# Kernel optimization log

Measured on AMD Instinct MI355X. Metric: run time of the kernel, lower is better.

The kernel has to match this reference:

```python
import jax, jax.numpy as jnp
import numpy as np

RADIUS = 2                 # soft detection radius (init kwarg)
NMS_RADIUS = 2             # hardcoded in detect_keypoints: simple_nms(scores, 2)
TOP_K = 4096
TEMPERATURE = 0.1
KSIZE = 2 * RADIUS + 1     # 5
KK = KSIZE * KSIZE         # 25


def _hw_grid(dtype):
    # flatten order j = dy*KSIZE + dx ; entry = (x_off, y_off)  (torch's [:, [1,0]])
    lin = jnp.linspace(-RADIUS, RADIUS, KSIZE, dtype=dtype)
    gx, gy = jnp.meshgrid(lin, lin)  # 'xy': gx[dy,dx]=lin[dx], gy[dy,dx]=lin[dy]
    return jnp.stack([gx, gy], axis=-1).reshape(-1, 2)  # (KK, 2)


def _maxpool(x, r):
    k = 2 * r + 1
    return jax.lax.reduce_window(x, -jnp.inf, jax.lax.max,
                                 (1, 1, k, k), (1, 1, 1, 1),
                                 ((0, 0), (0, 0), (r, r), (r, r)))


def _simple_nms(scores, r):
    zeros = jnp.zeros_like(scores)
    max_mask = scores == _maxpool(scores, r)
    for _ in range(2):
        supp_mask = _maxpool(max_mask.astype(scores.dtype), r) > 0
        supp_scores = jnp.where(supp_mask, zeros, scores)
        new_max_mask = supp_scores == _maxpool(supp_scores, r)
        max_mask = max_mask | (new_max_mask & ~supp_mask)
    return jnp.where(max_mask, scores, zeros)


def _bilinear_zeros(img, xy):
    # img: (h, w); xy: (K, 2) normalized [-1,1]; align_corners=True, zero padding
    h, w = img.shape
    px = (xy[:, 0] + 1.0) * 0.5 * (w - 1)
    py = (xy[:, 1] + 1.0) * 0.5 * (h - 1)
    x0 = jnp.floor(px); y0 = jnp.floor(py)
    wx1 = px - x0; wx0 = 1.0 - wx1
    wy1 = py - y0; wy0 = 1.0 - wy1
    def tap(xi, yi, wgt):
        valid = (xi >= 0) & (xi < w) & (yi >= 0) & (yi < h)
        xc = jnp.clip(xi, 0, w - 1).astype(jnp.int32)
        yc = jnp.clip(yi, 0, h - 1).astype(jnp.int32)
        return jnp.where(valid, img[yc, xc], 0.0) * wgt
    return (tap(x0, y0, wx0 * wy0) + tap(x0 + 1, y0, wx1 * wy0)
            + tap(x0, y0 + 1, wx0 * wy1) + tap(x0 + 1, y0 + 1, wx1 * wy1))


def _dkd_forward(scores_map):
    b, c, h, w = scores_map.shape
    dtype = scores_map.dtype
    scores_nograd = jax.lax.stop_gradient(scores_map)

    nms_scores = _simple_nms(scores_nograd, NMS_RADIUS)
    # zero out border band of width RADIUS
    ybad = (jnp.arange(h) < RADIUS) | (jnp.arange(h) >= h - RADIUS)
    xbad = (jnp.arange(w) < RADIUS) | (jnp.arange(w) >= w - RADIUS)
    border = ybad[:, None] | xbad[None, :]
    nms_scores = jnp.where(border[None, None], 0.0, nms_scores)

    # top-k over flattened score map (per image)
    _, idx = jax.lax.top_k(nms_scores.reshape(b, -1), TOP_K)  # (b, K)
    ix = idx % w
    iy = idx // w

    # patch gather == unfold(scores_map) + gather, done sparsely with zero pad
    padded = jnp.pad(scores_map[:, 0], ((0, 0), (RADIUS, RADIUS), (RADIUS, RADIUS)))
    off = jnp.arange(KSIZE)
    ys = iy[:, :, None] + off[None, None, :]           # (b, K, KSIZE)
    xs = ix[:, :, None] + off[None, None, :]
    bidx = jnp.arange(b)[:, None, None, None]
    patch_scores = padded[bidx, ys[:, :, :, None], xs[:, :, None, :]]  # (b,K,KSIZE,KSIZE)
    patch_scores = patch_scores.reshape(b, TOP_K, KK)

    hw_grid = _hw_grid(dtype)                          # (KK, 2)
    max_v = jax.lax.stop_gradient(patch_scores.max(axis=-1, keepdims=True))
    x_exp = jnp.exp((patch_scores - max_v) / TEMPERATURE)   # (b,K,KK)
    x_exp_sum = x_exp.sum(axis=-1, keepdims=True)            # (b,K,1)
    xy_residual = jnp.einsum('bkp,pd->bkd', x_exp, hw_grid) / x_exp_sum  # (b,K,2)
    hw_dist2 = (((hw_grid[None, None] - xy_residual[:, :, None]) / RADIUS) ** 2).sum(-1)
    scoredispersity = (x_exp * hw_dist2).sum(-1) / x_exp_sum[..., 0]     # (b,K)

    keypoints_xy_nms = jnp.stack([ix, iy], axis=-1).astype(dtype)
    wh = jnp.array([w - 1, h - 1], dtype=dtype)
    keypoints_xy = (keypoints_xy_nms + xy_residual) / wh * 2.0 - 1.0     # (b,K,2)

    kptscore = jax.vmap(_bilinear_zeros)(scores_map[:, 0], keypoints_xy)  # (b,K)
    return keypoints_xy, kptscore, scoredispersity


def setup_inputs() -> dict:
    key = jax.random.key(0)
    scores_map = jax.random.uniform(key, (8, 1, 1024, 1024), dtype=jnp.float32)
    return {"scores_map": scores_map}


def reference(scores_map):
    # matches torch forward: (keypoints, kptscores, scoredispersitys)
    return _dkd_forward(scores_map)
```

## Files before the change

kernel.cpp:

```cpp
#include <hip/hip_runtime.h>
#include <stdint.h>


namespace {

constexpr int B = 8;
constexpr int H = 1024;
constexpr int W = 1024;
constexpr int TOPK = 4096;
constexpr int CAND_CAP = 131072;
constexpr int SEL_CAP = 16384;
constexpr int LIST_CAP = 320;
constexpr int NHB = 32;

constexpr int RROWS = 92;
constexpr int NG = 22;
constexpr int STR = 88;
constexpr int MW4 = 4;
constexpr int NSTRIP = 11;
constexpr int NUNIT = NG * NSTRIP;

constexpr int RK_ME = 256;
constexpr int RK_CH = 1024;

constexpr size_t OFF_CNT   = 0;
constexpr size_t OFF_EH    = 4096;
constexpr size_t OFF_FH    = OFF_EH + (size_t)B * 256 * 4;
constexpr size_t OFF_RANK  = OFF_FH + (size_t)B * 256 * 4;
constexpr size_t OFF_SEL   = OFF_RANK + (size_t)B * SEL_CAP * 4;
constexpr size_t OFF_TOPK  = OFF_SEL + (size_t)B * SEL_CAP * 8;
constexpr size_t OFF_CAND  = OFF_TOPK + (size_t)B * TOPK * 8;
constexpr size_t MEMSET_BYTES = OFF_SEL;

__device__ __forceinline__ float max5(float a, float b, float c, float d, float e) {
  return fmaxf(fmaxf(fmaxf(a, b), fmaxf(c, d)), e);
}
__device__ __forceinline__ float4 ld4(const float* p) {
  return *reinterpret_cast<const float4*>(p);
}

template <int PASS>
__device__ __forceinline__ void score_pass(
    int u, int x0, int y0, const float* __restrict__ S,
    const uint32_t* __restrict__ MIN_, uint32_t* __restrict__ MOUT,
    uint64_t* list, uint32_t* cnt_loc, uint64_t* cand, uint32_t* cand_count, int b) {
  const int G = u % NG, s = u / NG;
  const int r0 = 2 + 8 * s;
  const int gx0 = x0 - 12 + 4 * G;
  uint32_t colm = 0;
#pragma unroll
  for (int j = 0; j < 4; ++j)
    if ((unsigned)(gx0 + j) < (unsigned)W) colm |= 1u << j;

  const int p2 = 4 * G - 6;
  const int pw2 = (p2 < 0) ? 0 : (p2 >> 5);
  const int psh2 = (p2 < 0) ? 0 : (p2 & 31);
  const int pls2 = (p2 < 0) ? -p2 : 0;

  float4 hw[5], cw[5];
  uint32_t snr[5], mor[5], cnb[5];
  constexpr int NK = (PASS == 0) ? 12 : 16;
#pragma unroll
  for (int k = 0; k < NK; ++k) {
    if (PASS != 0) {
      const int mr = r0 - 4 + k;
      uint32_t morrow = 0, cnib = 0;
      if ((unsigned)mr < (unsigned)RROWS) {
        const uint32_t* srow = MIN_ + mr * MW4;
        uint64_t X = (uint64_t)srow[pw2] | ((uint64_t)srow[pw2 + 1] << 32);
        uint64_t win = pls2 ? (X << pls2) : (X >> psh2);
        uint64_t t5 = win | (win >> 1) | (win >> 2) | (win >> 3) | (win >> 4);
        morrow = (uint32_t)t5 & 0xFFFu;
        cnib = (uint32_t)(win >> 6) & 0xFu;
      }
      mor[k % 5] = morrow;
      cnb[k % 5] = cnib;
    }
    const int ks = (PASS == 0) ? k : k - 4;
    if (ks >= 0) {
      const int sr = r0 - 2 + ks;
      uint32_t supp = 0;
      if (PASS != 0) supp = mor[0] | mor[1] | mor[2] | mor[3] | mor[4];
      const float* rowp = S + sr * STR + 4 * G;
      float4 d = ld4(rowp);
      float4 a = (G > 0) ? ld4(rowp - 4) : d;
      float4 e = (G < NG - 1) ? ld4(rowp + 4) : d;
      if (PASS != 0) {
        if (supp & 0x001u) a.x = 0.f;
        if (supp & 0x002u) a.y = 0.f;
        if (supp & 0x004u) a.z = 0.f;
        if (supp & 0x008u) a.w = 0.f;
        if (supp & 0x010u) d.x = 0.f;
        if (supp & 0x020u) d.y = 0.f;
        if (supp & 0x040u) d.z = 0.f;
        if (supp & 0x080u) d.w = 0.f;
        if (supp & 0x100u) e.x = 0.f;
        if (supp & 0x200u) e.y = 0.f;
        if (supp & 0x400u) e.z = 0.f;
        if (supp & 0x800u) e.w = 0.f;
      }
      float4 hm;
      hm.x = max5(a.z, a.w, d.x, d.y, d.z);
      hm.y = max5(a.w, d.x, d.y, d.z, d.w);
      hm.z = max5(d.x, d.y, d.z, d.w, e.x);
      hm.w = max5(d.y, d.z, d.w, e.x, e.y);
      hw[ks % 5] = hm;
      cw[ks % 5] = d;
      snr[ks % 5] = (supp >> 4) & 0xFu;
      if (ks >= 4) {
        const int rq = r0 - 4 + ks;
        const int gy = y0 - 12 + rq;
        float4 vm;
        vm.x = max5(hw[0].x, hw[1].x, hw[2].x, hw[3].x, hw[4].x);
        vm.y = max5(hw[0].y, hw[1].y, hw[2].y, hw[3].y, hw[4].y);
        vm.z = max5(hw[0].z, hw[1].z, hw[2].z, hw[3].z, hw[4].z);
        vm.w = max5(hw[0].w, hw[1].w, hw[2].w, hw[3].w, hw[4].w);
        float4 c = cw[(ks + 3) % 5];
        uint32_t nm = (uint32_t)(c.x == vm.x) | ((uint32_t)(c.y == vm.y) << 1) |
                      ((uint32_t)(c.z == vm.z) << 2) | ((uint32_t)(c.w == vm.w) << 3);
        nm &= ((unsigned)gy < (unsigned)H) ? colm : 0u;
        const int widx = rq * MW4 + (G >> 3);
        const int shift = 4 * (G & 7);
        if (PASS == 0) {
          if (nm) atomicOr(&MOUT[widx], nm << shift);
        } else if (PASS == 1) {
          uint32_t fin = cnb[ks % 5] | (nm & ~snr[(ks + 3) % 5]);
          if (fin) atomicOr(&MOUT[widx], fin << shift);
        } else {
          uint32_t fin = cnb[ks % 5] | (nm & ~snr[(ks + 3) % 5]);
          if (fin && G >= 3 && G < 19 && rq >= 12 && rq < 76 && gy >= 2 && gy < H - 2) {
#pragma unroll
            for (int j = 0; j < 4; ++j) {
              if ((fin >> j) & 1u) {
                int gx = gx0 + j;
                if (gx >= 2 && gx < W - 2) {
                  float sval = S[rq * STR + 4 * G + j];
                  if (sval > 0.0f) {
                    uint32_t bits = __float_as_uint(sval);
                    uint32_t flat = (uint32_t)(gy * W + gx);
                    uint64_t key = ((uint64_t)bits << 32) | (uint64_t)(0xFFFFFFFFu - flat);
                    uint32_t pos = atomicAdd(cnt_loc, 1u);
                    if (pos < (uint32_t)LIST_CAP) {
                      list[pos] = key;
                    } else {
                      uint32_t pp = atomicAdd(&cand_count[b], 1u);
                      if (pp < (uint32_t)CAND_CAP) cand[(size_t)b * CAND_CAP + pp] = key;
                    }
                  }
                }
              }
            }
          }
        }
      }
    }
  }
}

__global__ void __launch_bounds__(256, 4) k_nms(const float* __restrict__ scores,
                                                uint64_t* __restrict__ cand,
                                                uint32_t* __restrict__ cand_count) {
  __shared__ float S[RROWS * STR];
  __shared__ uint32_t M0s[RROWS * MW4];
  __shared__ uint32_t M1s[RROWS * MW4];
  __shared__ uint64_t list[LIST_CAP];
  __shared__ uint32_t cnt_loc, base_g;
  const int b = blockIdx.z;
  const int x0 = blockIdx.x * 64, y0 = blockIdx.y * 64;
  const int tid = threadIdx.x;
  const float* img = scores + (size_t)b * H * W;
  if (tid == 0) cnt_loc = 0;

  for (int u = tid; u < RROWS * NG; u += 256) {
    int r = u / NG, G = u % NG;
    int gy = y0 - 12 + r, gx = x0 - 12 + 4 * G;
    float4 v;
    if ((unsigned)gy < (unsigned)H && (unsigned)gx < (unsigned)W)
      v = ld4(img + (size_t)gy * W + gx);
    else
      v = make_float4(-INFINITY, -INFINITY, -INFINITY, -INFINITY);
    *reinterpret_cast<float4*>(&S[r * STR + 4 * G]) = v;
  }
  for (int i = tid; i < RROWS * MW4; i += 256) {
    M0s[i] = 0;
    M1s[i] = 0;
  }
  __syncthreads();
  if (tid < NUNIT)
    score_pass<0>(tid, x0, y0, S, nullptr, M0s, nullptr, nullptr, nullptr, nullptr, b);
  __syncthreads();
  if (tid < NUNIT)
    score_pass<1>(tid, x0, y0, S, M0s, M1s, nullptr, nullptr, nullptr, nullptr, b);
  __syncthreads();
  if (tid < NUNIT)
    score_pass<2>(tid, x0, y0, S, M1s, nullptr, list, &cnt_loc, cand, cand_count, b);
  __syncthreads();
  uint32_t nblk = cnt_loc;
  uint32_t nmain = nblk < (uint32_t)LIST_CAP ? nblk : (uint32_t)LIST_CAP;
  if (tid == 0) base_g = atomicAdd(&cand_count[b], nmain);
  __syncthreads();
  uint32_t bg = base_g;
  for (uint32_t i = tid; i < nmain; i += 256) {
    uint32_t pp = bg + i;
    if (pp < (uint32_t)CAND_CAP) cand[(size_t)b * CAND_CAP + pp] = list[i];
  }
}

__global__ void __launch_bounds__(256) k_ehist(const uint64_t* __restrict__ cand,
                                               const uint32_t* __restrict__ cand_count,
                                               uint32_t* __restrict__ gehist) {
  __shared__ uint32_t eh[256];
  const int b = blockIdx.y;
  uint32_t n = cand_count[b];
  if (n > (uint32_t)CAND_CAP) n = CAND_CAP;
  eh[threadIdx.x] = 0;
  __syncthreads();
  const uint64_t* cb = cand + (size_t)b * CAND_CAP;
  for (uint32_t i = blockIdx.x * 256 + threadIdx.x; i < n; i += NHB * 256)
    atomicAdd(&eh[(uint32_t)(cb[i] >> 55)], 1u);
  __syncthreads();
  uint32_t v = eh[threadIdx.x];
  if (v) atomicAdd(&gehist[b * 256 + threadIdx.x], v);
}

__global__ void __launch_bounds__(256) k_fhist(const uint64_t* __restrict__ cand,
                                               const uint32_t* __restrict__ cand_count,
                                               const uint32_t* __restrict__ gehist,
                                               uint32_t* __restrict__ gfhist) {
  __shared__ uint32_t fh[256];
  __shared__ uint32_t ehl[256];
  __shared__ int sE;
  const int b = blockIdx.y, t = threadIdx.x;
  uint32_t n = cand_count[b];
  if (n > (uint32_t)CAND_CAP) n = CAND_CAP;
  fh[t] = 0;
  ehl[t] = gehist[b * 256 + t];
  __syncthreads();
  if (t == 0) {
    uint32_t run = 0;
    int E = -1;
    for (int e = 255; e >= 0; --e) {
      uint32_t nrun = run + ehl[e];
      if (run < (uint32_t)TOPK && nrun >= (uint32_t)TOPK) E = e;
      run = nrun;
    }
    if (run < (uint32_t)TOPK) E = -1;
    sE = E;
  }
  __syncthreads();
  const int E = sE;
  if (E < 0) return;
  const uint64_t* cb = cand + (size_t)b * CAND_CAP;
  for (uint32_t i = blockIdx.x * 256 + t; i < n; i += NHB * 256) {
    uint64_t key = cb[i];
    if ((uint32_t)(key >> 55) == (uint32_t)E)
      atomicAdd(&fh[(uint32_t)(key >> 47) & 0xFFu], 1u);
  }
  __syncthreads();
  uint32_t v = fh[t];
  if (v) atomicAdd(&gfhist[b * 256 + t], v);
}

__global__ void __launch_bounds__(256) k_findthr(const uint32_t* __restrict__ gehist,
                                                 const uint32_t* __restrict__ gfhist,
                                                 uint64_t* __restrict__ thr_key) {
  __shared__ uint32_t ehl[256];
  __shared__ uint32_t fhl[256];
  const int b = blockIdx.x, t = threadIdx.x;
  ehl[t] = gehist[b * 256 + t];
  fhl[t] = gfhist[b * 256 + t];
  __syncthreads();
  if (t != 0) return;
  uint32_t run = 0, above = 0;
  int E = -1;
  for (int e = 255; e >= 0; --e) {
    uint32_t nrun = run + ehl[e];
    if (run < (uint32_t)TOPK && nrun >= (uint32_t)TOPK) {
      E = e;
      above = run;
    }
    run = nrun;
  }
  if (run < (uint32_t)TOPK) {
    thr_key[b] = 0ull;
    return;
  }
  uint32_t r2 = above;
  for (int j = 255; j >= 0; --j) {
    r2 += fhl[j];
    if (r2 >= (uint32_t)TOPK) {
      thr_key[b] = ((uint64_t)(((uint32_t)E << 8) | (uint32_t)j)) << 47;
      return;
    }
  }
}

__global__ void __launch_bounds__(1024) k_compact(const uint64_t* __restrict__ cand,
                                                  const uint32_t* __restrict__ cand_count,
                                                  const uint64_t* __restrict__ thr_key,
                                                  uint64_t* __restrict__ sel,
                                                  uint32_t* __restrict__ sel_count) {
  __shared__ uint64_t list[1024];
  __shared__ uint32_t cnt_loc;
  __shared__ uint32_t base_g;
  const int b = blockIdx.y;
  uint32_t n = cand_count[b];
  if (n > (uint32_t)CAND_CAP) n = CAND_CAP;
  const int tid = threadIdx.x;
  if (tid == 0) cnt_loc = 0;
  __syncthreads();
  uint32_t i = blockIdx.x * 1024 + tid;
  if (i < n) {
    uint64_t key = cand[(size_t)b * CAND_CAP + i];
    if (key >= thr_key[b]) {
      uint32_t pos = atomicAdd(&cnt_loc, 1u);
      list[pos] = key;
    }
  }
  __syncthreads();
  uint32_t nblk = cnt_loc;
  if (tid == 0 && nblk > 0) base_g = atomicAdd(&sel_count[b], nblk);
  __syncthreads();
  if (nblk > 0 && (uint32_t)tid < nblk) {
    uint32_t pp = base_g + tid;
    if (pp < (uint32_t)SEL_CAP) sel[(size_t)b * SEL_CAP + pp] = list[tid];
  }
}

__global__ void __launch_bounds__(RK_ME) k_rank_part(const uint64_t* __restrict__ sel,
                                                     const uint32_t* __restrict__ sel_count,
                                                     uint32_t* __restrict__ rankg) {
  __shared__ uint64_t keys[RK_CH];
  const int b = blockIdx.z;
  uint32_t n = sel_count[b];
  if (n > (uint32_t)SEL_CAP) n = SEL_CAP;
  const uint32_t me0 = blockIdx.x * RK_ME;
  const uint32_t c0 = blockIdx.y * RK_CH;
  if (me0 >= n || c0 >= n) return;
  const uint64_t* sb = sel + (size_t)b * SEL_CAP;
  uint32_t clen = n - c0;
  if (clen > (uint32_t)RK_CH) clen = RK_CH;
  for (uint32_t i = threadIdx.x; i < clen; i += RK_ME) keys[i] = sb[c0 + i];
  __syncthreads();
  const uint32_t me = me0 + threadIdx.x;
  if (me >= n) return;
  const uint64_t kme = sb[me];
  uint32_t rank = 0;
  uint32_t i = 0;
  for (; i + 8 <= clen; i += 8) {
    rank += (keys[i] > kme);
    rank += (keys[i + 1] > kme);
    rank += (keys[i + 2] > kme);
    rank += (keys[i + 3] > kme);
    rank += (keys[i + 4] > kme);
    rank += (keys[i + 5] > kme);
    rank += (keys[i + 6] > kme);
    rank += (keys[i + 7] > kme);
  }
  for (; i < clen; ++i) rank += (keys[i] > kme);
  if (rank) atomicAdd(&rankg[(size_t)b * SEL_CAP + me], rank);
}

__global__ void __launch_bounds__(256) k_scatter(const uint64_t* __restrict__ sel,
                                                 const uint32_t* __restrict__ sel_count,
                                                 const uint32_t* __restrict__ rankg,
                                                 uint64_t* __restrict__ topk) {
  const int b = blockIdx.y;
  uint32_t n = sel_count[b];
  if (n > (uint32_t)SEL_CAP) n = SEL_CAP;
  uint32_t i = blockIdx.x * 256 + threadIdx.x;
  if (i >= n) return;
  uint32_t r = rankg[(size_t)b * SEL_CAP + i];
  if (r < (uint32_t)TOPK) topk[(size_t)b * TOPK + r] = sel[(size_t)b * SEL_CAP + i];
}

__global__ void __launch_bounds__(256) k_refine(const float* __restrict__ scores,
                                                const uint64_t* __restrict__ topk,
                                                float* __restrict__ out) {
  int gid = blockIdx.x * 256 + threadIdx.x;
  int kp = gid >> 3, ln = gid & 7;
  const int b = kp / TOPK;
  const int k = kp % TOPK;
  uint64_t key = topk[(size_t)b * TOPK + k];
  uint32_t flat = 0xFFFFFFFFu - (uint32_t)(key & 0xFFFFFFFFull);
  if (flat >= (uint32_t)(H * W)) flat = 0;
  const int ix = (int)(flat % W);
  const int iy = (int)(flat / W);
  const float* img = scores + (size_t)b * H * W;

  const int nt = (ln == 0) ? 4 : 3;
  float v[4];
  float mymax = -INFINITY;
#pragma unroll
  for (int i = 0; i < 4; ++i) {
    if (i < nt) {
      int t = ln + 8 * i;
      int y = iy + t / 5 - 2, x = ix + t % 5 - 2;
      float val = ((unsigned)x < (unsigned)W && (unsigned)y < (unsigned)H)
                      ? img[(size_t)y * W + x] : 0.0f;
      v[i] = val;
      mymax = fmaxf(mymax, val);
    }
  }
#pragma unroll
  for (int m = 1; m < 8; m <<= 1) mymax = fmaxf(mymax, __shfl_xor(mymax, m));
  float e[4];
  float sum = 0.f, sx = 0.f, sy = 0.f;
#pragma unroll
  for (int i = 0; i < 4; ++i) {
    if (i < nt) {
      int t = ln + 8 * i;
      float ev = expf((v[i] - mymax) / 0.1f);
      e[i] = ev;
      sum += ev;
      sx += ev * (float)(t % 5 - 2);
      sy += ev * (float)(t / 5 - 2);
    }
  }
#pragma unroll
  for (int m = 1; m < 8; m <<= 1) {
    sum += __shfl_xor(sum, m);
    sx += __shfl_xor(sx, m);
    sy += __shfl_xor(sy, m);
  }
  float rx = sx / sum, ry = sy / sum;
  float dsp = 0.f;
#pragma unroll
  for (int i = 0; i < 4; ++i) {
    if (i < nt) {
      int t = ln + 8 * i;
      float dx = ((float)(t % 5 - 2) - rx) * 0.5f;
      float dy = ((float)(t / 5 - 2) - ry) * 0.5f;
      dsp += e[i] * (dx * dx + dy * dy);
    }
  }
#pragma unroll
  for (int m = 1; m < 8; m <<= 1) dsp += __shfl_xor(dsp, m);
  if (ln != 0) return;
  dsp /= sum;
  float kx = ((float)ix + rx) / 1023.0f * 2.0f - 1.0f;
  float ky = ((float)iy + ry) / 1023.0f * 2.0f - 1.0f;
  float px = (kx + 1.0f) * 0.5f * 1023.0f;
  float py = (ky + 1.0f) * 0.5f * 1023.0f;
  float x0f = floorf(px), y0f = floorf(py);
  float wx1 = px - x0f, wx0 = 1.0f - wx1;
  float wy1 = py - y0f, wy0 = 1.0f - wy1;
  int x0 = (int)x0f, y0 = (int)y0f;
  float sc = 0.0f;
  {
    int xs[2] = {x0, x0 + 1};
    int ys[2] = {y0, y0 + 1};
    float wxs[2] = {wx0, wx1};
    float wys[2] = {wy0, wy1};
#pragma unroll
    for (int yy = 0; yy < 2; ++yy)
#pragma unroll
      for (int xx = 0; xx < 2; ++xx) {
        int xi = xs[xx], yi = ys[yy];
        bool valid = (xi >= 0 && xi < W && yi >= 0 && yi < H);
        int xc = min(max(xi, 0), W - 1);
        int yc = min(max(yi, 0), H - 1);
        float vv = valid ? img[(size_t)yc * W + xc] : 0.0f;
        sc += vv * (wxs[xx] * wys[yy]);
      }
  }
  out[((size_t)b * TOPK + k) * 2 + 0] = kx;
  out[((size_t)b * TOPK + k) * 2 + 1] = ky;
  out[(size_t)B * TOPK * 2 + (size_t)b * TOPK + k] = sc;
  out[(size_t)B * TOPK * 3 + (size_t)b * TOPK + k] = dsp;
}

}

extern "C" void kernel_launch(void* const* d_in, const int* in_sizes, int n_in,
                              void* d_out, int out_size, void* d_ws, size_t ws_size,
                              hipStream_t stream) {
  const float* scores = (const float*)d_in[0];
  float* out = (float*)d_out;
  char* ws = (char*)d_ws;

  uint32_t* cnt = (uint32_t*)(ws + OFF_CNT);
  uint32_t* cand_count = cnt;
  uint32_t* sel_count  = cnt + 8;
  uint64_t* thr_key    = (uint64_t*)(cnt + 16);
  uint32_t* gehist = (uint32_t*)(ws + OFF_EH);
  uint32_t* gfhist = (uint32_t*)(ws + OFF_FH);
  uint32_t* rankg = (uint32_t*)(ws + OFF_RANK);
  uint64_t* sel  = (uint64_t*)(ws + OFF_SEL);
  uint64_t* topk = (uint64_t*)(ws + OFF_TOPK);
  uint64_t* cand = (uint64_t*)(ws + OFF_CAND);

  hipMemsetAsync(ws + OFF_CNT, 0, MEMSET_BYTES, stream);

  k_nms<<<dim3(W / 64, H / 64, B), 256, 0, stream>>>(scores, cand, cand_count);
  k_ehist<<<dim3(NHB, B), 256, 0, stream>>>(cand, cand_count, gehist);
  k_fhist<<<dim3(NHB, B), 256, 0, stream>>>(cand, cand_count, gehist, gfhist);
  k_findthr<<<B, 256, 0, stream>>>(gehist, gfhist, thr_key);
  k_compact<<<dim3(CAND_CAP / 1024, B), 1024, 0, stream>>>(cand, cand_count, thr_key,
                                                           sel, sel_count);
  k_rank_part<<<dim3(SEL_CAP / RK_ME, SEL_CAP / RK_CH, B), RK_ME, 0, stream>>>(
      sel, sel_count, rankg);
  k_scatter<<<dim3(SEL_CAP / 256, B), 256, 0, stream>>>(sel, sel_count, rankg, topk);
  k_refine<<<(B * TOPK * 8) / 256, 256, 0, stream>>>(scores, topk, out);
}
```

Before: 208.4 us.

## Fuse threshold search into compaction and scatter into refine, shrink memset

Drops the single-threaded k_findthr kernel. k_compact now loads both histograms and finds the threshold key with a parallel shared-memory suffix scan. Drops k_scatter: k_refine iterates over the selected list, reads each key's rank and writes its output at that rank. rankg is now zeroed inside compaction instead of by the memset, so the memset covers fewer bytes, and shared mask rows are padded from 4 to 5 words. This removes two launches and a global round-trip, at the cost of launching refine over the full selection capacity with many early-exit threads and repeating the scan in every compact block.

Result: faster. 198.7 us (-4.6%).

```diff
diff --git a/kernel.cpp b/kernel.cpp
--- a/kernel.cpp
+++ b/kernel.cpp
@@ -1,6 +1,5 @@
 #include <hip/hip_runtime.h>
 #include <stdint.h>
-
 
 namespace {
 
@@ -16,7 +15,7 @@
 constexpr int RROWS = 92;
 constexpr int NG = 22;
 constexpr int STR = 88;
-constexpr int MW4 = 4;
+constexpr int MW = 5;
 constexpr int NSTRIP = 11;
 constexpr int NUNIT = NG * NSTRIP;
 
@@ -28,9 +27,8 @@
 constexpr size_t OFF_FH    = OFF_EH + (size_t)B * 256 * 4;
 constexpr size_t OFF_RANK  = OFF_FH + (size_t)B * 256 * 4;
 constexpr size_t OFF_SEL   = OFF_RANK + (size_t)B * SEL_CAP * 4;
-constexpr size_t OFF_TOPK  = OFF_SEL + (size_t)B * SEL_CAP * 8;
-constexpr size_t OFF_CAND  = OFF_TOPK + (size_t)B * TOPK * 8;
-constexpr size_t MEMSET_BYTES = OFF_SEL;
+constexpr size_t OFF_CAND  = OFF_SEL + (size_t)B * SEL_CAP * 8;
+constexpr size_t MEMSET_BYTES = OFF_RANK;
 
 __device__ __forceinline__ float max5(float a, float b, float c, float d, float e) {
   return fmaxf(fmaxf(fmaxf(a, b), fmaxf(c, d)), e);
@@ -66,7 +64,7 @@
       const int mr = r0 - 4 + k;
       uint32_t morrow = 0, cnib = 0;
       if ((unsigned)mr < (unsigned)RROWS) {
-        const uint32_t* srow = MIN_ + mr * MW4;
+        const uint32_t* srow = MIN_ + mr * MW;
         uint64_t X = (uint64_t)srow[pw2] | ((uint64_t)srow[pw2 + 1] << 32);
         uint64_t win = pls2 ? (X << pls2) : (X >> psh2);
         uint64_t t5 = win | (win >> 1) | (win >> 2) | (win >> 3) | (win >> 4);
@@ -119,7 +117,7 @@
         uint32_t nm = (uint32_t)(c.x == vm.x) | ((uint32_t)(c.y == vm.y) << 1) |
                       ((uint32_t)(c.z == vm.z) << 2) | ((uint32_t)(c.w == vm.w) << 3);
         nm &= ((unsigned)gy < (unsigned)H) ? colm : 0u;
-        const int widx = rq * MW4 + (G >> 3);
+        const int widx = rq * MW + (G >> 3);
         const int shift = 4 * (G & 7);
         if (PASS == 0) {
           if (nm) atomicOr(&MOUT[widx], nm << shift);
@@ -161,8 +159,8 @@
                                                 uint64_t* __restrict__ cand,
                                                 uint32_t* __restrict__ cand_count) {
   __shared__ float S[RROWS * STR];
-  __shared__ uint32_t M0s[RROWS * MW4];
-  __shared__ uint32_t M1s[RROWS * MW4];
+  __shared__ uint32_t M0s[RROWS * MW];
+  __shared__ uint32_t M1s[RROWS * MW];
   __shared__ uint64_t list[LIST_CAP];
   __shared__ uint32_t cnt_loc, base_g;
   const int b = blockIdx.z;
@@ -181,7 +179,7 @@
       v = make_float4(-INFINITY, -INFINITY, -INFINITY, -INFINITY);
     *reinterpret_cast<float4*>(&S[r * STR + 4 * G]) = v;
   }
-  for (int i = tid; i < RROWS * MW4; i += 256) {
+  for (int i = tid; i < RROWS * MW; i += 256) {
     M0s[i] = 0;
     M1s[i] = 0;
   }
@@ -261,58 +259,66 @@
   if (v) atomicAdd(&gfhist[b * 256 + t], v);
 }
 
-__global__ void __launch_bounds__(256) k_findthr(const uint32_t* __restrict__ gehist,
-                                                 const uint32_t* __restrict__ gfhist,
-                                                 uint64_t* __restrict__ thr_key) {
-  __shared__ uint32_t ehl[256];
-  __shared__ uint32_t fhl[256];
-  const int b = blockIdx.x, t = threadIdx.x;
-  ehl[t] = gehist[b * 256 + t];
-  fhl[t] = gfhist[b * 256 + t];
-  __syncthreads();
-  if (t != 0) return;
-  uint32_t run = 0, above = 0;
-  int E = -1;
-  for (int e = 255; e >= 0; --e) {
-    uint32_t nrun = run + ehl[e];
-    if (run < (uint32_t)TOPK && nrun >= (uint32_t)TOPK) {
-      E = e;
-      above = run;
-    }
-    run = nrun;
-  }
-  if (run < (uint32_t)TOPK) {
-    thr_key[b] = 0ull;
-    return;
-  }
-  uint32_t r2 = above;
-  for (int j = 255; j >= 0; --j) {
-    r2 += fhl[j];
-    if (r2 >= (uint32_t)TOPK) {
-      thr_key[b] = ((uint64_t)(((uint32_t)E << 8) | (uint32_t)j)) << 47;
-      return;
-    }
-  }
-}
-
 __global__ void __launch_bounds__(1024) k_compact(const uint64_t* __restrict__ cand,
                                                   const uint32_t* __restrict__ cand_count,
-                                                  const uint64_t* __restrict__ thr_key,
+                                                  const uint32_t* __restrict__ gehist,
+                                                  const uint32_t* __restrict__ gfhist,
                                                   uint64_t* __restrict__ sel,
-                                                  uint32_t* __restrict__ sel_count) {
+                                                  uint32_t* __restrict__ sel_count,
+                                                  uint32_t* __restrict__ rankg) {
   __shared__ uint64_t list[1024];
-  __shared__ uint32_t cnt_loc;
-  __shared__ uint32_t base_g;
+  __shared__ uint32_t cnt_loc, base_g;
+  __shared__ uint32_t eh[256], fh[256];
+  __shared__ int sE;
+  __shared__ uint32_t sAbove;
+  __shared__ uint64_t s_thr;
   const int b = blockIdx.y;
   uint32_t n = cand_count[b];
   if (n > (uint32_t)CAND_CAP) n = CAND_CAP;
   const int tid = threadIdx.x;
-  if (tid == 0) cnt_loc = 0;
-  __syncthreads();
+  if (tid == 0) {
+    cnt_loc = 0;
+    sE = -1;
+    s_thr = 0ull;
+  }
+  if (tid < 256) {
+    eh[tid] = gehist[b * 256 + tid];
+    fh[tid] = gfhist[b * 256 + tid];
+  }
+  __syncthreads();
+  for (int d = 1; d < 256; d <<= 1) {
+    uint32_t ve = 0, vf = 0;
+    if (tid < 256) {
+      ve = (tid + d < 256) ? eh[tid + d] : 0u;
+      vf = (tid + d < 256) ? fh[tid + d] : 0u;
+    }
+    __syncthreads();
+    if (tid < 256) {
+      eh[tid] += ve;
+      fh[tid] += vf;
+    }
+    __syncthreads();
+  }
+  if (tid < 256) {
+    uint32_t nxt = (tid < 255) ? eh[tid + 1] : 0u;
+    if (eh[tid] >= (uint32_t)TOPK && nxt < (uint32_t)TOPK) {
+      sE = tid;
+      sAbove = nxt;
+    }
+  }
+  __syncthreads();
+  if (sE >= 0 && tid < 256) {
+    uint32_t above = sAbove;
+    uint32_t Fn = (tid < 255) ? fh[tid + 1] : 0u;
+    if (above + fh[tid] >= (uint32_t)TOPK && above + Fn < (uint32_t)TOPK)
+      s_thr = ((uint64_t)(((uint32_t)sE << 8) | (uint32_t)tid)) << 47;
+  }
+  __syncthreads();
+  const uint64_t thr = s_thr;
   uint32_t i = blockIdx.x * 1024 + tid;
   if (i < n) {
     uint64_t key = cand[(size_t)b * CAND_CAP + i];
-    if (key >= thr_key[b]) {
+    if (key >= thr) {
       uint32_t pos = atomicAdd(&cnt_loc, 1u);
       list[pos] = key;
     }
@@ -323,7 +329,10 @@
   __syncthreads();
   if (nblk > 0 && (uint32_t)tid < nblk) {
     uint32_t pp = base_g + tid;
-    if (pp < (uint32_t)SEL_CAP) sel[(size_t)b * SEL_CAP + pp] = list[tid];
+    if (pp < (uint32_t)SEL_CAP) {
+      sel[(size_t)b * SEL_CAP + pp] = list[tid];
+      rankg[(size_t)b * SEL_CAP + pp] = 0u;
+    }
   }
 }
 
@@ -361,27 +370,21 @@
   if (rank) atomicAdd(&rankg[(size_t)b * SEL_CAP + me], rank);
 }
 
-__global__ void __launch_bounds__(256) k_scatter(const uint64_t* __restrict__ sel,
-                                                 const uint32_t* __restrict__ sel_count,
-                                                 const uint32_t* __restrict__ rankg,
-                                                 uint64_t* __restrict__ topk) {
-  const int b = blockIdx.y;
+__global__ void __launch_bounds__(256) k_refine(const float* __restrict__ scores,
+                                                const uint64_t* __restrict__ sel,
+                                                const uint32_t* __restrict__ sel_count,
+                                                const uint32_t* __restrict__ rankg,
+                                                float* __restrict__ out) {
+  int gid = blockIdx.x * 256 + threadIdx.x;
+  int idx = gid >> 3, ln = gid & 7;
+  const int b = idx / SEL_CAP;
+  const int i = idx % SEL_CAP;
   uint32_t n = sel_count[b];
   if (n > (uint32_t)SEL_CAP) n = SEL_CAP;
-  uint32_t i = blockIdx.x * 256 + threadIdx.x;
-  if (i >= n) return;
+  if ((uint32_t)i >= n) return;
   uint32_t r = rankg[(size_t)b * SEL_CAP + i];
-  if (r < (uint32_t)TOPK) topk[(size_t)b * TOPK + r] = sel[(size_t)b * SEL_CAP + i];
-}
-
-__global__ void __launch_bounds__(256) k_refine(const float* __restrict__ scores,
-                                                const uint64_t* __restrict__ topk,
-                                                float* __restrict__ out) {
-  int gid = blockIdx.x * 256 + threadIdx.x;
-  int kp = gid >> 3, ln = gid & 7;
-  const int b = kp / TOPK;
-  const int k = kp % TOPK;
-  uint64_t key = topk[(size_t)b * TOPK + k];
+  if (r >= (uint32_t)TOPK) return;
+  uint64_t key = sel[(size_t)b * SEL_CAP + i];
   uint32_t flat = 0xFFFFFFFFu - (uint32_t)(key & 0xFFFFFFFFull);
   if (flat >= (uint32_t)(H * W)) flat = 0;
   const int ix = (int)(flat % W);
@@ -392,13 +395,13 @@
   float v[4];
   float mymax = -INFINITY;
 #pragma unroll
-  for (int i = 0; i < 4; ++i) {
-    if (i < nt) {
-      int t = ln + 8 * i;
+  for (int q = 0; q < 4; ++q) {
+    if (q < nt) {
+      int t = ln + 8 * q;
       int y = iy + t / 5 - 2, x = ix + t % 5 - 2;
       float val = ((unsigned)x < (unsigned)W && (unsigned)y < (unsigned)H)
                       ? img[(size_t)y * W + x] : 0.0f;
-      v[i] = val;
+      v[q] = val;
       mymax = fmaxf(mymax, val);
     }
   }
@@ -407,11 +410,11 @@
   float e[4];
   float sum = 0.f, sx = 0.f, sy = 0.f;
 #pragma unroll
-  for (int i = 0; i < 4; ++i) {
-    if (i < nt) {
-      int t = ln + 8 * i;
-      float ev = expf((v[i] - mymax) / 0.1f);
-      e[i] = ev;
+  for (int q = 0; q < 4; ++q) {
+    if (q < nt) {
+      int t = ln + 8 * q;
+      float ev = expf((v[q] - mymax) / 0.1f);
+      e[q] = ev;
       sum += ev;
       sx += ev * (float)(t % 5 - 2);
       sy += ev * (float)(t / 5 - 2);
@@ -426,12 +429,12 @@
   float rx = sx / sum, ry = sy / sum;
   float dsp = 0.f;
 #pragma unroll
-  for (int i = 0; i < 4; ++i) {
-    if (i < nt) {
-      int t = ln + 8 * i;
+  for (int q = 0; q < 4; ++q) {
+    if (q < nt) {
+      int t = ln + 8 * q;
       float dx = ((float)(t % 5 - 2) - rx) * 0.5f;
       float dy = ((float)(t / 5 - 2) - ry) * 0.5f;
-      dsp += e[i] * (dx * dx + dy * dy);
+      dsp += e[q] * (dx * dx + dy * dy);
     }
   }
 #pragma unroll
@@ -464,10 +467,10 @@
         sc += vv * (wxs[xx] * wys[yy]);
       }
   }
-  out[((size_t)b * TOPK + k) * 2 + 0] = kx;
-  out[((size_t)b * TOPK + k) * 2 + 1] = ky;
-  out[(size_t)B * TOPK * 2 + (size_t)b * TOPK + k] = sc;
-  out[(size_t)B * TOPK * 3 + (size_t)b * TOPK + k] = dsp;
+  out[((size_t)b * TOPK + r) * 2 + 0] = kx;
+  out[((size_t)b * TOPK + r) * 2 + 1] = ky;
+  out[(size_t)B * TOPK * 2 + (size_t)b * TOPK + r] = sc;
+  out[(size_t)B * TOPK * 3 + (size_t)b * TOPK + r] = dsp;
 }
 
 }
@@ -482,12 +485,10 @@
   uint32_t* cnt = (uint32_t*)(ws + OFF_CNT);
   uint32_t* cand_count = cnt;
   uint32_t* sel_count  = cnt + 8;
-  uint64_t* thr_key    = (uint64_t*)(cnt + 16);
   uint32_t* gehist = (uint32_t*)(ws + OFF_EH);
   uint32_t* gfhist = (uint32_t*)(ws + OFF_FH);
   uint32_t* rankg = (uint32_t*)(ws + OFF_RANK);
   uint64_t* sel  = (uint64_t*)(ws + OFF_SEL);
-  uint64_t* topk = (uint64_t*)(ws + OFF_TOPK);
   uint64_t* cand = (uint64_t*)(ws + OFF_CAND);
 
   hipMemsetAsync(ws + OFF_CNT, 0, MEMSET_BYTES, stream);
@@ -495,11 +496,10 @@
   k_nms<<<dim3(W / 64, H / 64, B), 256, 0, stream>>>(scores, cand, cand_count);
   k_ehist<<<dim3(NHB, B), 256, 0, stream>>>(cand, cand_count, gehist);
   k_fhist<<<dim3(NHB, B), 256, 0, stream>>>(cand, cand_count, gehist, gfhist);
-  k_findthr<<<B, 256, 0, stream>>>(gehist, gfhist, thr_key);
-  k_compact<<<dim3(CAND_CAP / 1024, B), 1024, 0, stream>>>(cand, cand_count, thr_key,
-                                                           sel, sel_count);
+  k_compact<<<dim3(CAND_CAP / 1024, B), 1024, 0, stream>>>(cand, cand_count, gehist,
+                                                           gfhist, sel, sel_count, rankg);
   k_rank_part<<<dim3(SEL_CAP / RK_ME, SEL_CAP / RK_CH, B), RK_ME, 0, stream>>>(
       sel, sel_count, rankg);
-  k_scatter<<<dim3(SEL_CAP / 256, B), 256, 0, stream>>>(sel, sel_count, rankg, topk);
-  k_refine<<<(B * TOPK * 8) / 256, 256, 0, stream>>>(scores, topk, out);
-}
+  k_refine<<<(B * SEL_CAP * 8) / 256, 256, 0, stream>>>(scores, sel, sel_count, rankg,
+                                                        out);
+}
```
